# Optimization experiments

Hardware: AMD Instinct MI355X
Metric: run time of the kernel (lower is better)

Reference implementation:

```python
import jax, jax.numpy as jnp
import numpy as np
import math

NUM_HEADS = 16
NUM_BUCKETS = 32
MAX_DISTANCE = 128


def _relative_position_bucket(relative_position, num_buckets=NUM_BUCKETS, max_distance=MAX_DISTANCE):
    num_buckets = num_buckets // 2
    ret = (relative_position >= 0).astype(jnp.int32) * num_buckets
    n = jnp.abs(relative_position)
    max_exact = num_buckets // 2
    is_small = n < max_exact
    # guard log(0); masked by is_small anyway
    n_safe = jnp.maximum(n, 1).astype(jnp.float32)
    val_if_large = max_exact + (
        jnp.log(n_safe / max_exact) / math.log(max_distance / max_exact) * (num_buckets - max_exact)
    ).astype(jnp.int32)
    val_if_large = jnp.minimum(val_if_large, num_buckets - 1)
    return ret + jnp.where(is_small, n, val_if_large)


def compute_bias(rel_bias, query_length, key_length):
    ctx = jnp.arange(query_length)[:, None]
    mem = jnp.arange(key_length)[None, :]
    rp = mem - ctx  # [Q, K]
    bucket = _relative_position_bucket(rp)  # [Q, K]
    values = rel_bias[bucket]  # [Q, K, H]
    return jnp.transpose(values, (2, 0, 1))[None]  # [1, H, Q, K]


def setup_inputs() -> dict:
    key = jax.random.key(0)
    ks = jax.random.split(key, 6)
    B, S, D = 2, 2048, 1024
    sd = 1.0 / math.sqrt(D)
    return {
        "x": jax.random.normal(ks[0], (B, S, D), jnp.float32),
        "wq": jax.random.normal(ks[1], (D, D), jnp.float32) * sd,
        "wk": jax.random.normal(ks[2], (D, D), jnp.float32) * sd,
        "wv": jax.random.normal(ks[3], (D, D), jnp.float32) * sd,
        "wo": jax.random.normal(ks[4], (D, D), jnp.float32) * sd,
        "rel_bias": jax.random.normal(ks[5], (NUM_BUCKETS, NUM_HEADS), jnp.float32),
    }


def reference(x, wq, wk, wv, wo, rel_bias):
    B, S, _ = x.shape
    inner_dim = wq.shape[0]
    head_dim = inner_dim // NUM_HEADS
    # nn.Linear stores weight as [out, in]: y = x @ W^T
    q = (x @ wq.T).reshape(B, S, NUM_HEADS, head_dim).transpose(0, 2, 1, 3)
    k = (x @ wk.T).reshape(B, S, NUM_HEADS, head_dim).transpose(0, 2, 1, 3)
    v = (x @ wv.T).reshape(B, S, NUM_HEADS, head_dim).transpose(0, 2, 1, 3)
    scores = jnp.einsum('bhqd,bhkd->bhqk', q, k) / math.sqrt(head_dim)
    past_bias = compute_bias(rel_bias, S, S)  # [1, H, S, S]
    scores = scores + past_bias
    attn_weights = jax.nn.softmax(scores, axis=-1)
    attn_output = jnp.einsum('bhqk,bhkd->bhqd', attn_weights, v)
    attn_output = attn_output.transpose(0, 2, 1, 3).reshape(B, S, inner_dim)
    attn_output = attn_output @ wo.T
    return (attn_output, past_bias)
```

## Files before the change

kernel.cpp:

```cpp
#include <hip/hip_runtime.h>

typedef __bf16 bf16_t;
typedef __bf16 bf16x8 __attribute__((ext_vector_type(8)));
typedef float  f32x4  __attribute__((ext_vector_type(4)));

#define ASYNC16(g, l) __builtin_amdgcn_global_load_lds( \
    (const __attribute__((address_space(1))) void*)(g), \
    (__attribute__((address_space(3))) void*)(l), 16, 0, 0)

#define MFMA(a, b, c) __builtin_amdgcn_mfma_f32_16x16x32_bf16(a, b, c, 0, 0, 0)

__global__ __launch_bounds__(256) void cast_all(
    const float* __restrict__ x, const float* __restrict__ wq,
    const float* __restrict__ wk, const float* __restrict__ wv,
    const float* __restrict__ wo,
    bf16_t* __restrict__ xb, bf16_t* __restrict__ wqkvb, bf16_t* __restrict__ wob)
{
  int i4 = blockIdx.x * 256 + threadIdx.x;
  int base = i4 * 4;
  const float* src; bf16_t* dst;
  if (base < 4194304) { src = x + base; dst = xb + base; }
  else {
    int j = base - 4194304;
    int w = j >> 20, o = j & 1048575;
    if      (w == 0) { src = wq + o; dst = wqkvb + o; }
    else if (w == 1) { src = wk + o; dst = wqkvb + (1 << 20) + o; }
    else if (w == 2) { src = wv + o; dst = wqkvb + (2 << 20) + o; }
    else             { src = wo + o; dst = wob + o; }
  }
  float4 v = *(const float4*)src;
  union { bf16_t h[4]; uint2 u; } pk;
  pk.h[0] = (bf16_t)v.x; pk.h[1] = (bf16_t)v.y;
  pk.h[2] = (bf16_t)v.z; pk.h[3] = (bf16_t)v.w;
  *(uint2*)dst = pk.u;
}

__global__ void build_tbl(const float* __restrict__ rel_bias,
                          float* __restrict__ tblB, float* __restrict__ tblE)
{
  int i = blockIdx.x * 256 + threadIdx.x;
  if (i >= 4095 * 16) return;
  int rpi = i >> 4;
  int h = i & 15;
  int rp = rpi - 2047;
  int ret = rp >= 0 ? 16 : 0;
  int n = rp < 0 ? -rp : rp;
  int b;
  if (n < 8) b = ret + n;
  else {
    double v = 2.0 * (log2((double)n) - 3.0);
    int bi = 8 + (int)v;
    b = ret + (bi < 15 ? bi : 15);
  }
  float v = rel_bias[b * 16 + h];
  tblB[h * 4096 + rpi] = v;
  tblE[h * 4096 + rpi] = v * 1.4426950408889634f;
}

__global__ __launch_bounds__(256) void gemm_qkv(
    const bf16_t* __restrict__ A, const bf16_t* __restrict__ B,
    bf16_t* __restrict__ qk, bf16_t* __restrict__ vt)
{
  const int K = 1024;
  __shared__ bf16_t As[128 * 32];
  __shared__ bf16_t Bs[128 * 32];
  const int t = threadIdx.x;
  const int w = t >> 6, l = t & 63, ln = l & 15, quad = l >> 4;
  const int wm = (w & 1) * 64, wn = (w >> 1) * 64;
  const int m0 = blockIdx.x * 128, n0 = blockIdx.y * 128;

  f32x4 acc[4][4] = {};
  const int rA = t >> 2, c8 = (t & 3) * 8;
  const bf16_t* Ag = A + (size_t)(m0 + rA) * K + c8;
  const bf16_t* Bg = B + (size_t)(n0 + rA) * K + c8;
  const size_t K64 = (size_t)64 * K;
  bf16_t* As0 = &As[t * 8];  bf16_t* As1 = &As[2048 + t * 8];
  bf16_t* Bs0 = &Bs[t * 8];  bf16_t* Bs1 = &Bs[2048 + t * 8];

  for (int kt = 0; kt < K; kt += 32) {
    ASYNC16(Ag + kt,       As0);
    ASYNC16(Ag + kt + K64, As1);
    ASYNC16(Bg + kt,       Bs0);
    ASYNC16(Bg + kt + K64, Bs1);
    __syncthreads();
    bf16x8 a[4], b[4];
#pragma unroll
    for (int mi = 0; mi < 4; ++mi)
      a[mi] = *(const bf16x8*)&As[(wm + mi * 16 + ln) * 32 + quad * 8];
#pragma unroll
    for (int ni = 0; ni < 4; ++ni)
      b[ni] = *(const bf16x8*)&Bs[(wn + ni * 16 + ln) * 32 + quad * 8];
#pragma unroll
    for (int mi = 0; mi < 4; ++mi)
#pragma unroll
      for (int ni = 0; ni < 4; ++ni)
        acc[mi][ni] = MFMA(a[mi], b[ni], acc[mi][ni]);
    __syncthreads();
  }

  if (n0 >= 2048) {
#pragma unroll
    for (int mi = 0; mi < 4; ++mi)
#pragma unroll
      for (int ni = 0; ni < 4; ++ni) {
        int col = n0 + wn + ni * 16 + ln - 2048;
        int hh = col >> 6, dd = col & 63;
        int row = m0 + wm + mi * 16 + quad * 4;
        int bb = row >> 11, ss = row & 2047;
        union { bf16_t h4[4]; uint2 u; } pk;
#pragma unroll
        for (int j = 0; j < 4; ++j) pk.h4[j] = (bf16_t)acc[mi][ni][j];
        *(uint2*)&vt[((size_t)(bb * 16 + hh) * 64 + dd) * 2048 + ss] = pk.u;
      }
  } else {
#pragma unroll
    for (int mi = 0; mi < 4; ++mi)
#pragma unroll
      for (int ni = 0; ni < 4; ++ni) {
        int row = m0 + wm + mi * 16 + quad * 4;
        int col = n0 + wn + ni * 16 + ln;
#pragma unroll
        for (int j = 0; j < 4; ++j)
          qk[(size_t)(row + j) * 2048 + col] = (bf16_t)acc[mi][ni][j];
      }
  }
}

__global__ __launch_bounds__(256) void gemm_bt_f32(
    const bf16_t* __restrict__ A, const bf16_t* __restrict__ B,
    float* __restrict__ C, int M, int N, int K)
{
  __shared__ bf16_t As[128 * 32];
  __shared__ bf16_t Bs[128 * 32];
  const int t = threadIdx.x;
  const int w = t >> 6, l = t & 63, ln = l & 15, quad = l >> 4;
  const int wm = (w & 1) * 64, wn = (w >> 1) * 64;
  const int m0 = blockIdx.x * 128, n0 = blockIdx.y * 128;

  f32x4 acc[4][4] = {};
  const int rA = t >> 2, c8 = (t & 3) * 8;
  const bf16_t* Ag = A + (size_t)(m0 + rA) * K + c8;
  const bf16_t* Bg = B + (size_t)(n0 + rA) * K + c8;
  const size_t K64 = (size_t)64 * K;
  bf16_t* As0 = &As[t * 8];  bf16_t* As1 = &As[2048 + t * 8];
  bf16_t* Bs0 = &Bs[t * 8];  bf16_t* Bs1 = &Bs[2048 + t * 8];

  for (int kt = 0; kt < K; kt += 32) {
    ASYNC16(Ag + kt,       As0);
    ASYNC16(Ag + kt + K64, As1);
    ASYNC16(Bg + kt,       Bs0);
    ASYNC16(Bg + kt + K64, Bs1);
    __syncthreads();
    bf16x8 a[4], b[4];
#pragma unroll
    for (int mi = 0; mi < 4; ++mi)
      a[mi] = *(const bf16x8*)&As[(wm + mi * 16 + ln) * 32 + quad * 8];
#pragma unroll
    for (int ni = 0; ni < 4; ++ni)
      b[ni] = *(const bf16x8*)&Bs[(wn + ni * 16 + ln) * 32 + quad * 8];
#pragma unroll
    for (int mi = 0; mi < 4; ++mi)
#pragma unroll
      for (int ni = 0; ni < 4; ++ni)
        acc[mi][ni] = MFMA(a[mi], b[ni], acc[mi][ni]);
    __syncthreads();
  }

#pragma unroll
  for (int mi = 0; mi < 4; ++mi)
#pragma unroll
    for (int ni = 0; ni < 4; ++ni) {
      int row = m0 + wm + mi * 16 + quad * 4;
      int col = n0 + wn + ni * 16 + ln;
#pragma unroll
      for (int j = 0; j < 4; ++j)
        C[(size_t)(row + j) * N + col] = acc[mi][ni][j];
    }
}

__global__ __launch_bounds__(256) void flash_attn(
    const bf16_t* __restrict__ qk, const bf16_t* __restrict__ vt,
    const float* __restrict__ tblE, bf16_t* __restrict__ attn)
{
  __shared__ __align__(16) bf16_t Kt[128 * 72];
  __shared__ __align__(16) bf16_t Vs[64 * 136];
  __shared__ __align__(16) bf16_t Pt[4 * 16 * 136];
  const int t = threadIdx.x, w = t >> 6, l = t & 63, ln = l & 15, quad = l >> 4;
  const int q0 = blockIdx.x * 64, h = blockIdx.y, b = blockIdx.z;
  const int S = 2048;
  const int q = q0 + w * 16 + ln;

  const bf16_t* Qp = qk + (size_t)(b * S + q) * 2048 + h * 64 + quad * 8;
  bf16x8 bq0 = *(const bf16x8*)Qp;
  bf16x8 bq1 = *(const bf16x8*)(Qp + 32);

  f32x4 o[4] = {};
  float mi = -1e30f, li = 0.f;

  const bf16_t* Kg = qk + (size_t)(b * S) * 2048 + 1024 + h * 64;
  const bf16_t* Vg = vt + (size_t)(b * 16 + h) * 64 * 2048;
  const float* tb = tblE + h * 4096 + 2047 - q;

  const int kr = t >> 3, kc8 = (t & 7) * 8;
  const int dr = t >> 4, vc8 = (t & 15) * 8;

  for (int kt = 0; kt < S; kt += 128) {
    __syncthreads();
#pragma unroll
    for (int cc = 0; cc < 4; ++cc) {
      uint4 kv = *(const uint4*)(Kg + (size_t)(kt + kr + 32 * cc) * 2048 + kc8);
      uint4 vv = *(const uint4*)(Vg + (size_t)(dr + 16 * cc) * 2048 + kt + vc8);
      *(uint4*)&Kt[(kr + 32 * cc) * 72 + kc8] = kv;
      *(uint4*)&Vs[(dr + 16 * cc) * 136 + vc8] = vv;
    }
    __syncthreads();

    f32x4 xs[8];
    float tm = -1e30f;
    const float* tbk = tb + kt;
#pragma unroll
    for (int f = 0; f < 8; ++f) {
      const bf16_t* kp = &Kt[(f * 16 + ln) * 72 + quad * 8];
      bf16x8 a0 = *(const bf16x8*)kp;
      bf16x8 a1 = *(const bf16x8*)(kp + 32);
      f32x4 acc = {};
      acc = MFMA(a0, bq0, acc);
      acc = MFMA(a1, bq1, acc);
#pragma unroll
      for (int j = 0; j < 4; ++j) {
        float xv = fmaf(acc[j], 0.18033688011112042f,
                        __ldg(tbk + f * 16 + quad * 4 + j));
        xs[f][j] = xv;
        tm = fmaxf(tm, xv);
      }
    }
    tm = fmaxf(tm, __shfl_xor(tm, 16));
    tm = fmaxf(tm, __shfl_xor(tm, 32));
    float mn = fmaxf(mi, tm);
    float al = __builtin_amdgcn_exp2f(mi - mn);
    mi = mn;
    float rs = 0.f;
    bf16_t* pw = &Pt[w * 2176 + ln * 136];
#pragma unroll
    for (int f = 0; f < 8; ++f) {
      union { bf16_t h4[4]; uint2 u; } pk;
#pragma unroll
      for (int j = 0; j < 4; ++j) {
        float p = __builtin_amdgcn_exp2f(xs[f][j] - mn);
        rs += p;
        pk.h4[j] = (bf16_t)p;
      }
      *(uint2*)&pw[f * 16 + quad * 4] = pk.u;
    }
    rs += __shfl_xor(rs, 16);
    rs += __shfl_xor(rs, 32);
    li = li * al + rs;
#pragma unroll
    for (int dt = 0; dt < 4; ++dt)
#pragma unroll
      for (int j = 0; j < 4; ++j)
        o[dt][j] *= al;

#pragma unroll
    for (int kk = 0; kk < 4; ++kk) {
      bf16x8 bp = *(const bf16x8*)&Pt[w * 2176 + ln * 136 + kk * 32 + quad * 8];
#pragma unroll
      for (int dt = 0; dt < 4; ++dt) {
        bf16x8 av = *(const bf16x8*)&Vs[(dt * 16 + ln) * 136 + kk * 32 + quad * 8];
        o[dt] = MFMA(av, bp, o[dt]);
      }
    }
  }

  float inv = 1.f / li;
  bf16_t* op = attn + (size_t)(b * S + q) * 1024 + h * 64 + quad * 4;
#pragma unroll
  for (int dt = 0; dt < 4; ++dt) {
    union { bf16_t h4[4]; uint2 u; } pk;
#pragma unroll
    for (int j = 0; j < 4; ++j) pk.h4[j] = (bf16_t)(o[dt][j] * inv);
    *(uint2*)&op[dt * 16] = pk.u;
  }
}

__global__ __launch_bounds__(256) void bias_out(const float* __restrict__ tbl,
                                                float* __restrict__ out1)
{
  int i = blockIdx.x * 256 + threadIdx.x;
  int hq = i >> 9;
  int k4 = (i & 511) * 4;
  int h = hq >> 11, q = hq & 2047;
  const float* tp = tbl + (h << 12) + (k4 - q + 2047);
  float4 v;
  v.x = __ldg(tp);     v.y = __ldg(tp + 1);
  v.z = __ldg(tp + 2); v.w = __ldg(tp + 3);
  ((float4*)out1)[i] = v;
}

extern "C" void kernel_launch(void* const* d_in, const int* in_sizes, int n_in,
                              void* d_out, int out_size, void* d_ws, size_t ws_size,
                              hipStream_t stream)
{
  const float* x  = (const float*)d_in[0];
  const float* wq = (const float*)d_in[1];
  const float* wk = (const float*)d_in[2];
  const float* wv = (const float*)d_in[3];
  const float* wo = (const float*)d_in[4];
  const float* rb = (const float*)d_in[5];
  float* out0 = (float*)d_out;
  float* out1 = out0 + 4194304;

  char* ws = (char*)d_ws;
  bf16_t* xb    = (bf16_t*)(ws);
  bf16_t* wqkvb = (bf16_t*)(ws + 8388608);
  bf16_t* wob   = (bf16_t*)(ws + 14680064);
  bf16_t* qk    = (bf16_t*)(ws + 16777216);
  bf16_t* vt    = (bf16_t*)(ws + 33554432);
  float*  tblB  = (float*)(ws + 41943040);
  float*  tblE  = (float*)(ws + 42205184);
  bf16_t* attnb = xb;

  cast_all<<<8192, 256, 0, stream>>>(x, wq, wk, wv, wo, xb, wqkvb, wob);
  build_tbl<<<256, 256, 0, stream>>>(rb, tblB, tblE);
  gemm_qkv<<<dim3(32, 24), 256, 0, stream>>>(xb, wqkvb, qk, vt);
  flash_attn<<<dim3(32, 16, 2), 256, 0, stream>>>(qk, vt, tblE, attnb);
  gemm_bt_f32<<<dim3(32, 8), 256, 0, stream>>>(attnb, wob, out0, 4096, 1024, 1024);
  bias_out<<<65536, 256, 0, stream>>>(tblB, out1);
}
```

Before: 486.9 us.

## Prefetch next K/V tile into registers and alias P buffer onto K tile LDS

The flash attention loop now loads the next K/V tile from global memory into registers while the current tile is being computed, then writes them to LDS at the top of the next iteration. The separate P staging buffer is removed and P is written into the K tile region after an extra barrier, which cuts LDS use and allows a launch-bounds occupancy hint of 4 blocks. Bias loads are also vectorized into a single 4-wide load. The cost is extra registers for the prefetch and one more barrier per iteration.

```diff
diff --git a/kernel.cpp b/kernel.cpp
--- a/kernel.cpp
+++ b/kernel.cpp
@@ -3,6 +3,7 @@
 typedef __bf16 bf16_t;
 typedef __bf16 bf16x8 __attribute__((ext_vector_type(8)));
 typedef float  f32x4  __attribute__((ext_vector_type(4)));
+typedef float  f32x4u __attribute__((ext_vector_type(4), aligned(4)));
 
 #define ASYNC16(g, l) __builtin_amdgcn_global_load_lds( \
     (const __attribute__((address_space(1))) void*)(g), \
@@ -178,13 +179,12 @@
     }
 }
 
-__global__ __launch_bounds__(256) void flash_attn(
+__global__ __launch_bounds__(256, 4) void flash_attn(
     const bf16_t* __restrict__ qk, const bf16_t* __restrict__ vt,
     const float* __restrict__ tblE, bf16_t* __restrict__ attn)
 {
   __shared__ __align__(16) bf16_t Kt[128 * 72];
   __shared__ __align__(16) bf16_t Vs[64 * 136];
-  __shared__ __align__(16) bf16_t Pt[4 * 16 * 136];
   const int t = threadIdx.x, w = t >> 6, l = t & 63, ln = l & 15, quad = l >> 4;
   const int q0 = blockIdx.x * 64, h = blockIdx.y, b = blockIdx.z;
   const int S = 2048;
@@ -204,16 +204,28 @@
   const int kr = t >> 3, kc8 = (t & 7) * 8;
   const int dr = t >> 4, vc8 = (t & 15) * 8;
 
+  uint4 kreg[4], vreg[4];
+#pragma unroll
+  for (int cc = 0; cc < 4; ++cc) {
+    kreg[cc] = *(const uint4*)(Kg + (size_t)(kr + 32 * cc) * 2048 + kc8);
+    vreg[cc] = *(const uint4*)(Vg + (size_t)(dr + 16 * cc) * 2048 + vc8);
+  }
+
   for (int kt = 0; kt < S; kt += 128) {
     __syncthreads();
 #pragma unroll
     for (int cc = 0; cc < 4; ++cc) {
-      uint4 kv = *(const uint4*)(Kg + (size_t)(kt + kr + 32 * cc) * 2048 + kc8);
-      uint4 vv = *(const uint4*)(Vg + (size_t)(dr + 16 * cc) * 2048 + kt + vc8);
-      *(uint4*)&Kt[(kr + 32 * cc) * 72 + kc8] = kv;
-      *(uint4*)&Vs[(dr + 16 * cc) * 136 + vc8] = vv;
-    }
-    __syncthreads();
+      *(uint4*)&Kt[(kr + 32 * cc) * 72 + kc8] = kreg[cc];
+      *(uint4*)&Vs[(dr + 16 * cc) * 136 + vc8] = vreg[cc];
+    }
+    __syncthreads();
+    if (kt + 128 < S) {
+#pragma unroll
+      for (int cc = 0; cc < 4; ++cc) {
+        kreg[cc] = *(const uint4*)(Kg + (size_t)(kt + 128 + kr + 32 * cc) * 2048 + kc8);
+        vreg[cc] = *(const uint4*)(Vg + (size_t)(dr + 16 * cc) * 2048 + kt + 128 + vc8);
+      }
+    }
 
     f32x4 xs[8];
     float tm = -1e30f;
@@ -226,10 +238,10 @@
       f32x4 acc = {};
       acc = MFMA(a0, bq0, acc);
       acc = MFMA(a1, bq1, acc);
+      f32x4u bv = *(const f32x4u*)(tbk + f * 16 + quad * 4);
 #pragma unroll
       for (int j = 0; j < 4; ++j) {
-        float xv = fmaf(acc[j], 0.18033688011112042f,
-                        __ldg(tbk + f * 16 + quad * 4 + j));
+        float xv = fmaf(acc[j], 0.18033688011112042f, bv[j]);
         xs[f][j] = xv;
         tm = fmaxf(tm, xv);
       }
@@ -240,7 +252,9 @@
     float al = __builtin_amdgcn_exp2f(mi - mn);
     mi = mn;
     float rs = 0.f;
-    bf16_t* pw = &Pt[w * 2176 + ln * 136];
+
+    __syncthreads();
+    bf16_t* pw = &Kt[w * 2304 + ln * 136];
 #pragma unroll
     for (int f = 0; f < 8; ++f) {
       union { bf16_t h4[4]; uint2 u; } pk;
@@ -263,7 +277,7 @@
 
 #pragma unroll
     for (int kk = 0; kk < 4; ++kk) {
-      bf16x8 bp = *(const bf16x8*)&Pt[w * 2176 + ln * 136 + kk * 32 + quad * 8];
+      bf16x8 bp = *(const bf16x8*)&Kt[w * 2304 + ln * 136 + kk * 32 + quad * 8];
 #pragma unroll
       for (int dt = 0; dt < 4; ++dt) {
         bf16x8 av = *(const bf16x8*)&Vs[(dt * 16 + ln) * 136 + kk * 32 + quad * 8];
```

Result: slower. 553.7 us (+13.7%).
